# Optimization experiments

Measured on AMD Instinct MI355X. Metric: run time of the kernel, lower is better.

Reference implementation:

```python
import jax, jax.numpy as jnp
import numpy as np

LMBDA = 1.0  # init lmbda

def setup_inputs() -> dict:
    key = jax.random.key(0)
    k1, k2, k3 = jax.random.split(key, 3)
    N, P, M = 8, 4096, 2048
    x_hat = jax.random.normal(k1, (N, P, 3), dtype=jnp.float32)
    points = jax.random.normal(k2, (N, P, 3), dtype=jnp.float32)
    # likelihoods in (0, 1]; avoid log2(0)
    lik_y = jax.random.uniform(k3, (N, M), dtype=jnp.float32, minval=1e-6, maxval=1.0)
    return {"x_hat": x_hat, "points": points, "lik_y": lik_y}

def _chamfer(x, y):
    # x: [N,P,3], y: [N,Q,3] -> scalar bidirectional mean chamfer (squared L2)
    x2 = jnp.sum(x * x, axis=-1)                      # [N,P]
    y2 = jnp.sum(y * y, axis=-1)                      # [N,Q]
    xy = jnp.einsum('npc,nqc->npq', x, y)             # [N,P,Q]
    d = x2[:, :, None] + y2[None if False else slice(None), None, :] - 2.0 * xy  # [N,P,Q]
    d = x2[:, :, None] + y2[:, None, :] - 2.0 * xy    # [N,P,Q] squared distances
    cham_x = jnp.mean(jnp.min(d, axis=2))             # x -> nearest in y
    cham_y = jnp.mean(jnp.min(d, axis=1))             # y -> nearest in x
    return cham_x + cham_y

def reference(x_hat, points, lik_y):
    N, P, C = points.shape
    # bpp loss: sum log2(likelihood) / (-N) bits, normalized per point
    bit_y = jnp.sum(jnp.log2(lik_y)) / (-N)
    bpp_y = bit_y / P
    bit_loss = bit_y
    bpp_loss = bit_loss / P
    rec_loss = _chamfer(x_hat, points)
    loss = bpp_loss + LMBDA * rec_loss
    return loss, bpp_loss, rec_loss, bit_loss, bpp_y
```

## Files before the change

### kernel.cpp

```cpp
#include <hip/hip_runtime.h>
#include <math.h>

#define NB 8
#define PP 4096
#define MM 2048
#define DIRS 2

#define PCHUNK 1024
#define NPBLK  (PP / PCHUNK)
#define QSLICES 16
#define QS (PP / QSLICES)

#define NMIN (DIRS * NB * PP)

__device__ __forceinline__ unsigned fenc(float f) {
    unsigned u = __float_as_uint(f);
    return (u & 0x80000000u) ? ~u : (u | 0x80000000u);
}
__device__ __forceinline__ float fdec(unsigned k) {
    return __uint_as_float((k & 0x80000000u) ? (k & 0x7FFFFFFFu) : ~k);
}

__global__ void log2sum_kernel(const float* __restrict__ lik, float* __restrict__ wssum, int total) {
    int tid = blockIdx.x * blockDim.x + threadIdx.x;
    float s = 0.f;
    for (int i = tid; i < total; i += gridDim.x * blockDim.x)
        s += log2f(lik[i]);
    #pragma unroll
    for (int off = 32; off > 0; off >>= 1)
        s += __shfl_down(s, off, 64);
    __shared__ float red[4];
    int lane = threadIdx.x & 63, wid = threadIdx.x >> 6;
    if (lane == 0) red[wid] = s;
    __syncthreads();
    if (threadIdx.x == 0)
        atomicAdd(&wssum[2], red[0] + red[1] + red[2] + red[3]);
}

__global__ __launch_bounds__(256, 4) void chamfer_kernel(const float* __restrict__ x,
                                                         const float* __restrict__ y,
                                                         unsigned* __restrict__ wsmin) {
    int bx = blockIdx.x;
    int qs  = bx & (QSLICES - 1); bx >>= 4;
    int pc  = bx & (NPBLK - 1);   bx >>= 2;
    int n   = bx & 7;             bx >>= 3;
    int dir = bx;
    const float* a = dir ? y : x;
    const float* b = dir ? x : y;
    const float* an = a + (size_t)n * PP * 3;
    const float* bn = b + (size_t)n * PP * 3;

    __shared__ float4 lds[QS];
    int t = threadIdx.x;
    {
        int q = qs * QS + t;
        const float* bp = bn + (size_t)q * 3;
        float y0 = bp[0], y1 = bp[1], y2 = bp[2];
        lds[t] = make_float4(-2.f * y0, -2.f * y1, -2.f * y2,
                             y0 * y0 + y1 * y1 + y2 * y2);
    }

    float X0[4], X1[4], X2[4], XS[4], M[4];
    #pragma unroll
    for (int i = 0; i < 4; ++i) {
        int p = pc * PCHUNK + i * 256 + t;
        const float* ap = an + (size_t)p * 3;
        X0[i] = ap[0]; X1[i] = ap[1]; X2[i] = ap[2];
        XS[i] = X0[i] * X0[i] + X1[i] * X1[i] + X2[i] * X2[i];
        M[i] = INFINITY;
    }
    __syncthreads();

    #pragma unroll 4
    for (int q = 0; q < QS; ++q) {
        float4 v = lds[q];
        #pragma unroll
        for (int i = 0; i < 4; ++i) {
            float d = fmaf(X0[i], v.x, fmaf(X1[i], v.y, fmaf(X2[i], v.z, v.w)));
            M[i] = fminf(M[i], d);
        }
    }

    #pragma unroll
    for (int i = 0; i < 4; ++i) {
        int p = pc * PCHUNK + i * 256 + t;
        atomicMin(&wsmin[((size_t)dir * NB + n) * PP + p], fenc(M[i] + XS[i]));
    }
}

__global__ void reduce_kernel(const unsigned* __restrict__ wsmin, float* __restrict__ wssum) {
    int tid = blockIdx.x * blockDim.x + threadIdx.x;
    float s0 = 0.f, s1 = 0.f;
    for (int i = tid; i < NMIN; i += gridDim.x * blockDim.x) {
        float v = fdec(wsmin[i]);
        if (i < NB * PP) s0 += v; else s1 += v;
    }
    #pragma unroll
    for (int off = 32; off > 0; off >>= 1) {
        s0 += __shfl_down(s0, off, 64);
        s1 += __shfl_down(s1, off, 64);
    }
    __shared__ float r0[4], r1[4];
    int lane = threadIdx.x & 63, wid = threadIdx.x >> 6;
    if (lane == 0) { r0[wid] = s0; r1[wid] = s1; }
    __syncthreads();
    if (threadIdx.x == 0) {
        atomicAdd(&wssum[0], r0[0] + r0[1] + r0[2] + r0[3]);
        atomicAdd(&wssum[1], r1[0] + r1[1] + r1[2] + r1[3]);
    }
}

__global__ void finalize_kernel(const float* __restrict__ wssum, float* __restrict__ out) {
    if (threadIdx.x == 0) {
        float cham_x = wssum[0] / (float)(NB * PP);
        float cham_y = wssum[1] / (float)(NB * PP);
        float rec = cham_x + cham_y;
        float bit_y = wssum[2] / (-(float)NB);
        float bpp = bit_y / (float)PP;
        out[0] = bpp + 1.0f * rec;
        out[1] = bpp;
        out[2] = rec;
        out[3] = bit_y;
        out[4] = bpp;
    }
}

extern "C" void kernel_launch(void* const* d_in, const int* in_sizes, int n_in,
                              void* d_out, int out_size, void* d_ws, size_t ws_size,
                              hipStream_t stream) {
    const float* x_hat  = (const float*)d_in[0];
    const float* points = (const float*)d_in[1];
    const float* lik    = (const float*)d_in[2];
    float* out = (float*)d_out;
    unsigned* wsmin = (unsigned*)d_ws;
    float* wssum = (float*)d_ws + NMIN;

    hipMemsetAsync(wsmin, 0xFF, NMIN * sizeof(unsigned), stream);
    hipMemsetAsync(wssum, 0, 3 * sizeof(float), stream);
    log2sum_kernel<<<32, 256, 0, stream>>>(lik, wssum, NB * MM);
    chamfer_kernel<<<DIRS * NB * NPBLK * QSLICES, 256, 0, stream>>>(x_hat, points, wsmin);
    reduce_kernel<<<64, 256, 0, stream>>>(wsmin, wssum);
    finalize_kernel<<<1, 64, 0, stream>>>(wssum, out);
}
```

Measured before the change: 40.14 us.

## Replace atomicMin with per-slice partial planes and fuse reductions into one kernel

The chamfer kernel now writes per-Q-slice partial minima to separate planes instead of doing encoded atomicMin into one buffer, which removes a large memset and the atomic contention. A single reduce kernel takes the min across the 16 planes, also computes the log2 likelihood sum, and finalizes the outputs in the last block through a completion counter. This drops two kernel launches and one memset. In exchange it uses about 16x more workspace traffic for the partials, and the inner loop is unrolled by two Q points.

```diff
diff --git a/kernel.cpp b/kernel.cpp
--- a/kernel.cpp
+++ b/kernel.cpp
@@ -5,45 +5,20 @@
 #define PP 4096
 #define MM 2048
 #define DIRS 2
-
-#define PCHUNK 1024
-#define NPBLK  (PP / PCHUNK)
 #define QSLICES 16
 #define QS (PP / QSLICES)
-
+#define PCHUNK 1024
+#define NPBLK (PP / PCHUNK)
 #define NMIN (DIRS * NB * PP)
-
-__device__ __forceinline__ unsigned fenc(float f) {
-    unsigned u = __float_as_uint(f);
-    return (u & 0x80000000u) ? ~u : (u | 0x80000000u);
-}
-__device__ __forceinline__ float fdec(unsigned k) {
-    return __uint_as_float((k & 0x80000000u) ? (k & 0x7FFFFFFFu) : ~k);
-}
-
-__global__ void log2sum_kernel(const float* __restrict__ lik, float* __restrict__ wssum, int total) {
-    int tid = blockIdx.x * blockDim.x + threadIdx.x;
-    float s = 0.f;
-    for (int i = tid; i < total; i += gridDim.x * blockDim.x)
-        s += log2f(lik[i]);
-    #pragma unroll
-    for (int off = 32; off > 0; off >>= 1)
-        s += __shfl_down(s, off, 64);
-    __shared__ float red[4];
-    int lane = threadIdx.x & 63, wid = threadIdx.x >> 6;
-    if (lane == 0) red[wid] = s;
-    __syncthreads();
-    if (threadIdx.x == 0)
-        atomicAdd(&wssum[2], red[0] + red[1] + red[2] + red[3]);
-}
+#define NLIK (NB * MM)
 
 __global__ __launch_bounds__(256, 4) void chamfer_kernel(const float* __restrict__ x,
                                                          const float* __restrict__ y,
-                                                         unsigned* __restrict__ wsmin) {
+                                                         float* __restrict__ wspart) {
     int bx = blockIdx.x;
     int qs  = bx & (QSLICES - 1); bx >>= 4;
     int pc  = bx & (NPBLK - 1);   bx >>= 2;
-    int n   = bx & 7;             bx >>= 3;
+    int n   = bx & (NB - 1);      bx >>= 3;
     int dir = bx;
     const float* a = dir ? y : x;
     const float* b = dir ? x : y;
@@ -72,56 +47,67 @@
     __syncthreads();
 
     #pragma unroll 4
-    for (int q = 0; q < QS; ++q) {
-        float4 v = lds[q];
+    for (int q = 0; q < QS; q += 2) {
+        float4 v0 = lds[q];
+        float4 v1 = lds[q + 1];
         #pragma unroll
         for (int i = 0; i < 4; ++i) {
-            float d = fmaf(X0[i], v.x, fmaf(X1[i], v.y, fmaf(X2[i], v.z, v.w)));
-            M[i] = fminf(M[i], d);
+            float d0 = fmaf(X0[i], v0.x, fmaf(X1[i], v0.y, fmaf(X2[i], v0.z, v0.w)));
+            float d1 = fmaf(X0[i], v1.x, fmaf(X1[i], v1.y, fmaf(X2[i], v1.z, v1.w)));
+            M[i] = fminf(fminf(M[i], d0), d1);
         }
     }
 
+    float* plane = wspart + (size_t)qs * NMIN;
+    int slot = (dir * NB + n) * PP + pc * PCHUNK + t;
     #pragma unroll
-    for (int i = 0; i < 4; ++i) {
-        int p = pc * PCHUNK + i * 256 + t;
-        atomicMin(&wsmin[((size_t)dir * NB + n) * PP + p], fenc(M[i] + XS[i]));
-    }
+    for (int i = 0; i < 4; ++i)
+        plane[slot + i * 256] = M[i] + XS[i];
 }
 
-__global__ void reduce_kernel(const unsigned* __restrict__ wsmin, float* __restrict__ wssum) {
-    int tid = blockIdx.x * blockDim.x + threadIdx.x;
-    float s0 = 0.f, s1 = 0.f;
-    for (int i = tid; i < NMIN; i += gridDim.x * blockDim.x) {
-        float v = fdec(wsmin[i]);
-        if (i < NB * PP) s0 += v; else s1 += v;
-    }
+__global__ __launch_bounds__(256) void reduce_kernel(const float* __restrict__ wspart,
+                                                     const float* __restrict__ lik,
+                                                     float* __restrict__ wssum,
+                                                     float* __restrict__ out) {
+    int t = blockIdx.x * 256 + threadIdx.x;
+    float m = wspart[t];
+    #pragma unroll
+    for (int s = 1; s < QSLICES; ++s)
+        m = fminf(m, wspart[(size_t)s * NMIN + t]);
+
+    float l = 0.f;
+    if (t < NLIK) l = __log2f(lik[t]);
+
     #pragma unroll
     for (int off = 32; off > 0; off >>= 1) {
-        s0 += __shfl_down(s0, off, 64);
-        s1 += __shfl_down(s1, off, 64);
+        m += __shfl_down(m, off, 64);
+        l += __shfl_down(l, off, 64);
     }
-    __shared__ float r0[4], r1[4];
+    __shared__ float rm[4], rl[4];
     int lane = threadIdx.x & 63, wid = threadIdx.x >> 6;
-    if (lane == 0) { r0[wid] = s0; r1[wid] = s1; }
+    if (lane == 0) { rm[wid] = m; rl[wid] = l; }
     __syncthreads();
     if (threadIdx.x == 0) {
-        atomicAdd(&wssum[0], r0[0] + r0[1] + r0[2] + r0[3]);
-        atomicAdd(&wssum[1], r1[0] + r1[1] + r1[2] + r1[3]);
-    }
-}
-
-__global__ void finalize_kernel(const float* __restrict__ wssum, float* __restrict__ out) {
-    if (threadIdx.x == 0) {
-        float cham_x = wssum[0] / (float)(NB * PP);
-        float cham_y = wssum[1] / (float)(NB * PP);
-        float rec = cham_x + cham_y;
-        float bit_y = wssum[2] / (-(float)NB);
-        float bpp = bit_y / (float)PP;
-        out[0] = bpp + 1.0f * rec;
-        out[1] = bpp;
-        out[2] = rec;
-        out[3] = bit_y;
-        out[4] = bpp;
+        int dir = blockIdx.x >> 7;
+        atomicAdd(&wssum[dir], rm[0] + rm[1] + rm[2] + rm[3]);
+        if (blockIdx.x < 64)
+            atomicAdd(&wssum[2], rl[0] + rl[1] + rl[2] + rl[3]);
+        __threadfence();
+        unsigned done = atomicAdd((unsigned*)&wssum[3], 1u);
+        if (done == 255u) {
+            __threadfence();
+            float s0 = __hip_atomic_load(&wssum[0], __ATOMIC_ACQUIRE, __HIP_MEMORY_SCOPE_AGENT);
+            float s1 = __hip_atomic_load(&wssum[1], __ATOMIC_ACQUIRE, __HIP_MEMORY_SCOPE_AGENT);
+            float s2 = __hip_atomic_load(&wssum[2], __ATOMIC_ACQUIRE, __HIP_MEMORY_SCOPE_AGENT);
+            float rec = s0 / (float)(NB * PP) + s1 / (float)(NB * PP);
+            float bit_y = s2 / (-(float)NB);
+            float bpp = bit_y / (float)PP;
+            out[0] = bpp + 1.0f * rec;
+            out[1] = bpp;
+            out[2] = rec;
+            out[3] = bit_y;
+            out[4] = bpp;
+        }
     }
 }
 
@@ -132,13 +118,10 @@
     const float* points = (const float*)d_in[1];
     const float* lik    = (const float*)d_in[2];
     float* out = (float*)d_out;
-    unsigned* wsmin = (unsigned*)d_ws;
-    float* wssum = (float*)d_ws + NMIN;
+    float* wssum  = (float*)d_ws;
+    float* wspart = (float*)d_ws + 16;
 
-    hipMemsetAsync(wsmin, 0xFF, NMIN * sizeof(unsigned), stream);
-    hipMemsetAsync(wssum, 0, 3 * sizeof(float), stream);
-    log2sum_kernel<<<32, 256, 0, stream>>>(lik, wssum, NB * MM);
-    chamfer_kernel<<<DIRS * NB * NPBLK * QSLICES, 256, 0, stream>>>(x_hat, points, wsmin);
-    reduce_kernel<<<64, 256, 0, stream>>>(wsmin, wssum);
-    finalize_kernel<<<1, 64, 0, stream>>>(wssum, out);
+    hipMemsetAsync(wssum, 0, 16, stream);
+    chamfer_kernel<<<DIRS * NB * NPBLK * QSLICES, 256, 0, stream>>>(x_hat, points, wspart);
+    reduce_kernel<<<256, 256, 0, stream>>>(wspart, lik, wssum, out);
 }
```

Measured after the change: 41.48 us. 1.03x slower.
